# Kernel optimization log

Measured on AMD Instinct MI355X. Metric: run time of the kernel, lower is better.

Reference implementation:

```python
import jax, jax.numpy as jnp
import numpy as np

HEAD = 128
BLOCK = 16
MAX_POS = 32768


def _rope_cache(dim=HEAD, base=10000.0, max_pos=MAX_POS):
    # Mirrors PrecomputedRotaryEmbedding: inv_freq/t in bf16, then cos/sin.
    inv = (1.0 / base ** (jnp.arange(0, dim, 2, dtype=jnp.float32) / dim)).astype(jnp.bfloat16)
    t = jnp.arange(max_pos, dtype=jnp.bfloat16)
    freqs = t[:, None] * inv[None, :]                      # [P, dim/2]
    emb = jnp.concatenate([freqs, freqs], axis=-1)         # [P, dim]
    return jnp.cos(emb).astype(jnp.float32), jnp.sin(emb).astype(jnp.float32)


def _rotary(x, cos, sin):
    # x: [B, H, D], cos/sin: [B, D]
    d2 = x.shape[-1] // 2
    rot = jnp.concatenate([-x[..., d2:], x[..., :d2]], axis=-1)
    return x * cos[:, None, :] + rot * sin[:, None, :]


def setup_inputs() -> dict:
    key = jax.random.key(0)
    ks = jax.random.split(key, 8)
    B, H, Hkv, D = 32, 32, 8, 128
    blocks_per_seq, bs = 128, BLOCK
    nblk = B * blocks_per_seq
    query = jax.random.normal(ks[0], (B, H, D), dtype=jnp.float32)
    k_new = jax.random.normal(ks[1], (B, Hkv, D), dtype=jnp.float32)
    v_new = jax.random.normal(ks[2], (B, Hkv, D), dtype=jnp.float32)
    k_cache = jax.random.normal(ks[3], (nblk, bs, Hkv, D), dtype=jnp.float32)
    v_cache = jax.random.normal(ks[4], (nblk, bs, Hkv, D), dtype=jnp.float32)
    block_table = jnp.arange(nblk, dtype=jnp.int32).reshape(B, blocks_per_seq)
    context_lens = jax.random.randint(ks[5], (B,), 1, 2048, dtype=jnp.int32)
    return {"query": query, "key": k_new, "value": v_new,
            "k_cache": k_cache, "v_cache": v_cache,
            "block_table": block_table, "context_lens": context_lens}


def reference(query, key, value, k_cache, v_cache, block_table, context_lens):
    B, H, D = query.shape
    Hkv = key.shape[1]
    nblk, bs, _, _ = k_cache.shape
    max_ctx = block_table.shape[1] * bs

    cos_c, sin_c = _rope_cache(dim=D)
    pos = context_lens.astype(jnp.int32)
    cos, sin = cos_c[pos], sin_c[pos]                      # [B, D]
    q = _rotary(query, cos, sin)                           # [B, H, D]
    k_new = _rotary(key, cos, sin)                         # [B, Hkv, D]

    # Scatter new k/v into the paged cache at slot of token (ctx - 1).
    last = pos - 1
    slot = block_table[jnp.arange(B), last // bs] * bs + last % bs  # [B]
    kf = k_cache.reshape(nblk * bs, Hkv, D).at[slot].set(k_new)
    vf = v_cache.reshape(nblk * bs, Hkv, D).at[slot].set(value)

    # Gather per-sequence KV via block table (irregular paged access).
    t = jnp.arange(max_ctx)
    idx = block_table[:, t // bs].astype(jnp.int32) * bs + (t % bs)[None, :].astype(jnp.int32)  # [B, L]
    idx = jnp.clip(idx, 0, nblk * bs - 1)
    K = kf[idx]                                            # [B, L, Hkv, D]
    V = vf[idx]

    scale = D ** -0.5
    g = H // Hkv
    qg = q.reshape(B, Hkv, g, D)
    scores = jnp.einsum('bkgd,blkd->bkgl', qg, K) * scale  # [B, Hkv, g, L]
    valid = t[None, :] < pos[:, None]                      # [B, L]
    scores = jnp.where(valid[:, None, None, :], scores, -1e30)
    p = jax.nn.softmax(scores, axis=-1)
    out = jnp.einsum('bkgl,blkd->bkgd', p, V)              # [B, Hkv, g, D]
    return out.reshape(B, H, D)
```

## Files before the change

### kernel.cpp

```cpp
#include <hip/hip_runtime.h>
#include <hip/hip_bf16.h>
#include <math.h>

#define NB 32
#define NH 32
#define HKV 8
#define GQ 4
#define DH 128
#define BS 16
#define BPS 128
#define MAXC 2048
#define NSPLIT 8
#define TILE 32
#define PART_STRIDE 520

__device__ __forceinline__ float bf16r(float x) {
    return __bfloat162float(__float2bfloat16(x));
}

__global__ void rope_kernel(const float* __restrict__ q,
                            const float* __restrict__ knew,
                            const int* __restrict__ ctx,
                            float* __restrict__ q_rot,
                            float* __restrict__ k_rot)
{
    int b = blockIdx.x;
    int d = threadIdx.x;
    int pos = ctx[b];
    int i2 = d & 63;
    float e  = (float)i2 * (1.0f / 64.0f);
    float pf = (float)pow(10000.0, (double)e);
    float inv = bf16r(1.0f / pf);
    float tb  = bf16r((float)pos);
    float fr  = bf16r(tb * inv);
    float c   = bf16r(cosf(fr));
    float s   = bf16r(sinf(fr));

    const float* qb = q + (size_t)b * NH * DH;
    float* qo = q_rot + (size_t)b * NH * DH;
    #pragma unroll 4
    for (int h = 0; h < NH; ++h) {
        float x  = qb[h * DH + d];
        float xr = (d < 64) ? -qb[h * DH + d + 64] : qb[h * DH + d - 64];
        qo[h * DH + d] = x * c + xr * s;
    }
    const float* kb = knew + (size_t)b * HKV * DH;
    float* ko = k_rot + (size_t)b * HKV * DH;
    #pragma unroll
    for (int h = 0; h < HKV; ++h) {
        float x  = kb[h * DH + d];
        float xr = (d < 64) ? -kb[h * DH + d + 64] : kb[h * DH + d - 64];
        ko[h * DH + d] = x * c + xr * s;
    }
}

__global__ void rowidx_kernel(const int* __restrict__ bt,
                              const int* __restrict__ ctx,
                              int* __restrict__ rowidx)
{
    __shared__ int slot_l[NB];
    int tid = threadIdx.x;
    if (tid < NB) {
        int last = ctx[tid] - 1;
        slot_l[tid] = bt[tid * BPS + (last >> 4)] * BS + (last & 15);
    }
    __syncthreads();
    int g = blockIdx.x * 256 + tid;
    int b = g >> 11;
    int t = g & (MAXC - 1);
    int flat = bt[b * BPS + (t >> 4)] * BS + (t & 15);
    int o = flat;
    #pragma unroll
    for (int j = 0; j < NB; ++j)
        if (flat == slot_l[j]) o = -(j + 1);
    rowidx[g] = o;
}

__global__ __launch_bounds__(256) void attn_partial(
    const float* __restrict__ kc, const float* __restrict__ vc,
    const float* __restrict__ vnew,
    const int* __restrict__ ctx,
    const float* __restrict__ q_rot, const float* __restrict__ k_rot,
    const int* __restrict__ rowidx, float* __restrict__ part)
{
    __shared__ float q_lds[GQ][DH];
    __shared__ float k_lds[TILE][DH];
    __shared__ float v_lds[TILE][DH];
    __shared__ float p_lds[GQ][TILE];

    int tid = threadIdx.x;
    int bid = blockIdx.x;
    int sp  = bid & (NSPLIT - 1);
    int kvh = (bid / NSPLIT) & (HKV - 1);
    int b   = bid / (NSPLIT * HKV);

    int L = ctx[b];
    int chunk = (L + NSPLIT - 1) / NSPLIT;
    int start = sp * chunk;
    int end   = min(L, start + chunk);

    {
        const float* qs = q_rot + ((size_t)b * NH + kvh * GQ) * DH;
        ((float*)q_lds)[tid]       = qs[tid];
        ((float*)q_lds)[tid + 256] = qs[tid + 256];
    }

    int lane = tid & 63;
    int h    = tid >> 6;
    int l    = lane & 31;
    int half = lane >> 5;
    int rr   = tid >> 5;
    int c4   = tid & 31;

    float  m_run = -INFINITY;
    float  s_run = 0.0f;
    float2 acc   = make_float2(0.f, 0.f);

    float4 k0, k1, k2, k3, v0, v1, v2, v3;

#define GATHER(T, KD, VD)                                                   \
    {                                                                        \
        int tt = min((T), end - 1);                                          \
        int o  = rowidx[(b << 11) | tt];                                     \
        int j  = -o - 1;                                                     \
        const float* kp = (o >= 0) ? kc + (size_t)o * (HKV * DH) + kvh * DH  \
                                   : k_rot + ((size_t)j * HKV + kvh) * DH;   \
        const float* vp = (o >= 0) ? vc + (size_t)o * (HKV * DH) + kvh * DH  \
                                   : vnew + ((size_t)j * HKV + kvh) * DH;    \
        KD = ((const float4*)kp)[c4];                                        \
        VD = ((const float4*)vp)[c4];                                        \
    }

#define PREFETCH(TB)                    \
    GATHER((TB) + rr,      k0, v0);     \
    GATHER((TB) + rr + 8,  k1, v1);     \
    GATHER((TB) + rr + 16, k2, v2);     \
    GATHER((TB) + rr + 24, k3, v3);

#define LDS_WRITE(TB)                                                        \
    {                                                                        \
        if ((TB) + rr < end) {                                               \
            int sc = (c4 ^ rr) * 4;                                          \
            *(float4*)&k_lds[rr][sc] = k0; *(float4*)&v_lds[rr][sc] = v0;    \
        }                                                                    \
        if ((TB) + rr + 8 < end) {                                           \
            int sc = (c4 ^ (rr + 8)) * 4;                                    \
            *(float4*)&k_lds[rr + 8][sc] = k1; *(float4*)&v_lds[rr + 8][sc] = v1; \
        }                                                                    \
        if ((TB) + rr + 16 < end) {                                          \
            int sc = (c4 ^ (rr + 16)) * 4;                                   \
            *(float4*)&k_lds[rr + 16][sc] = k2; *(float4*)&v_lds[rr + 16][sc] = v2; \
        }                                                                    \
        if ((TB) + rr + 24 < end) {                                          \
            int sc = (c4 ^ (rr + 24)) * 4;                                   \
            *(float4*)&k_lds[rr + 24][sc] = k3; *(float4*)&v_lds[rr + 24][sc] = v3; \
        }                                                                    \
    }

    PREFETCH(start);
    __syncthreads();

    for (int t0 = start; t0 < end; t0 += TILE) {
        int n = min(TILE, end - t0);

        LDS_WRITE(t0);
        __syncthreads();

        PREFETCH(t0 + TILE);

        float s = 0.f;
        if (l < n) {
            const float4* qrow = (const float4*)q_lds[h];
            #pragma unroll
            for (int k = 0; k < 16; ++k) {
                int j = half * 16 + k;
                float4 a  = qrow[j];
                float4 bb = *(const float4*)&k_lds[l][(j ^ l) * 4];
                s += a.x * bb.x + a.y * bb.y + a.z * bb.z + a.w * bb.w;
            }
        }
        s += __shfl_xor(s, 32);
        s *= 0.08838834764831845f;

        float sm = (l < n) ? s : -INFINITY;
        float tm = sm;
        #pragma unroll
        for (int off = 16; off >= 1; off >>= 1)
            tm = fmaxf(tm, __shfl_xor(tm, off));
        float mnew = fmaxf(m_run, tm);
        float p  = (l < n) ? expf(s - mnew) : 0.f;
        float ts = p;
        #pragma unroll
        for (int off = 16; off >= 1; off >>= 1)
            ts += __shfl_xor(ts, off);
        float r = expf(m_run - mnew);
        s_run = s_run * r + ts;
        m_run = mnew;
        acc.x *= r; acc.y *= r;
        if (half == 0) p_lds[h][l] = p;

        int jc = lane >> 1, sub = lane & 1;
        for (int ll = 0; ll < n; ++ll) {
            float pv = p_lds[h][ll];
            const float2 vv = *(const float2*)&v_lds[ll][((jc ^ ll) << 2) + sub * 2];
            acc.x += pv * vv.x;
            acc.y += pv * vv.y;
        }
        __syncthreads();
    }

    float* pp = part + (size_t)bid * PART_STRIDE + h * 130;
    if (lane == 0) { pp[0] = m_run; pp[1] = s_run; }
    *(float2*)&pp[2 + lane * 2] = acc;
}

__global__ void reduce_kernel(const float* __restrict__ part,
                              float* __restrict__ out)
{
    int blk = blockIdx.x;
    int d   = threadIdx.x;
    int b   = blk >> 5;
    int hq  = blk & 31;
    int kvh = hq >> 2;
    int g   = hq & 3;
    const float* base = part + ((size_t)(b * HKV + kvh) * NSPLIT) * PART_STRIDE + g * 130;

    float M = -INFINITY;
    #pragma unroll
    for (int s = 0; s < NSPLIT; ++s)
        M = fmaxf(M, base[(size_t)s * PART_STRIDE]);
    float S = 0.f, o = 0.f;
    #pragma unroll
    for (int s = 0; s < NSPLIT; ++s) {
        float ms = base[(size_t)s * PART_STRIDE];
        float f  = expf(ms - M);
        S += base[(size_t)s * PART_STRIDE + 1] * f;
        o += base[(size_t)s * PART_STRIDE + 2 + d] * f;
    }
    out[(size_t)blk * DH + d] = o / S;
}

extern "C" void kernel_launch(void* const* d_in, const int* in_sizes, int n_in,
                              void* d_out, int out_size, void* d_ws, size_t ws_size,
                              hipStream_t stream)
{
    const float* q    = (const float*)d_in[0];
    const float* knew = (const float*)d_in[1];
    const float* vnew = (const float*)d_in[2];
    const float* kc   = (const float*)d_in[3];
    const float* vc   = (const float*)d_in[4];
    const int*   bt   = (const int*)d_in[5];
    const int*   ctx  = (const int*)d_in[6];
    float* out = (float*)d_out;

    float* ws     = (float*)d_ws;
    float* q_rot  = ws;
    float* k_rot  = ws + 131072;
    int*   rowidx = (int*)(ws + 131072 + 32768);
    float* part   = ws + 131072 + 32768 + 65536;

    rope_kernel<<<NB, 128, 0, stream>>>(q, knew, ctx, q_rot, k_rot);
    rowidx_kernel<<<NB * MAXC / 256, 256, 0, stream>>>(bt, ctx, rowidx);
    attn_partial<<<NB * HKV * NSPLIT, 256, 0, stream>>>(
        kc, vc, vnew, ctx, q_rot, k_rot, rowidx, part);
    reduce_kernel<<<NB * NH, 128, 0, stream>>>(part, out);
}
```

Measured before the change: 78.62 us.

## Fuse rope and rowidx kernels, double split count, shrink tiles, use nontemporal gathers

```diff
diff --git a/kernel.cpp b/kernel.cpp
--- a/kernel.cpp
+++ b/kernel.cpp
@@ -10,62 +10,34 @@
 #define BS 16
 #define BPS 128
 #define MAXC 2048
-#define NSPLIT 8
-#define TILE 32
-#define PART_STRIDE 520
+#define NSPLIT 16
+#define TILE 16
+#define HSTR 132
+#define PART_STRIDE (GQ * HSTR)
+
+typedef __attribute__((ext_vector_type(4))) float f32x4;
 
 __device__ __forceinline__ float bf16r(float x) {
     return __bfloat162float(__float2bfloat16(x));
 }
 
-__global__ void rope_kernel(const float* __restrict__ q,
+__global__ void prep_kernel(const float* __restrict__ q,
                             const float* __restrict__ knew,
+                            const int* __restrict__ bt,
                             const int* __restrict__ ctx,
                             float* __restrict__ q_rot,
-                            float* __restrict__ k_rot)
-{
-    int b = blockIdx.x;
-    int d = threadIdx.x;
-    int pos = ctx[b];
-    int i2 = d & 63;
-    float e  = (float)i2 * (1.0f / 64.0f);
-    float pf = (float)pow(10000.0, (double)e);
-    float inv = bf16r(1.0f / pf);
-    float tb  = bf16r((float)pos);
-    float fr  = bf16r(tb * inv);
-    float c   = bf16r(cosf(fr));
-    float s   = bf16r(sinf(fr));
-
-    const float* qb = q + (size_t)b * NH * DH;
-    float* qo = q_rot + (size_t)b * NH * DH;
-    #pragma unroll 4
-    for (int h = 0; h < NH; ++h) {
-        float x  = qb[h * DH + d];
-        float xr = (d < 64) ? -qb[h * DH + d + 64] : qb[h * DH + d - 64];
-        qo[h * DH + d] = x * c + xr * s;
-    }
-    const float* kb = knew + (size_t)b * HKV * DH;
-    float* ko = k_rot + (size_t)b * HKV * DH;
-    #pragma unroll
-    for (int h = 0; h < HKV; ++h) {
-        float x  = kb[h * DH + d];
-        float xr = (d < 64) ? -kb[h * DH + d + 64] : kb[h * DH + d - 64];
-        ko[h * DH + d] = x * c + xr * s;
-    }
-}
-
-__global__ void rowidx_kernel(const int* __restrict__ bt,
-                              const int* __restrict__ ctx,
-                              int* __restrict__ rowidx)
+                            float* __restrict__ k_rot,
+                            int* __restrict__ rowidx)
 {
     __shared__ int slot_l[NB];
-    int tid = threadIdx.x;
+    int tid = threadIdx.x, bid = blockIdx.x;
     if (tid < NB) {
         int last = ctx[tid] - 1;
         slot_l[tid] = bt[tid * BPS + (last >> 4)] * BS + (last & 15);
     }
     __syncthreads();
-    int g = blockIdx.x * 256 + tid;
+
+    int g = bid * 256 + tid;
     int b = g >> 11;
     int t = g & (MAXC - 1);
     int flat = bt[b * BPS + (t >> 4)] * BS + (t & 15);
@@ -74,9 +46,41 @@
     for (int j = 0; j < NB; ++j)
         if (flat == slot_l[j]) o = -(j + 1);
     rowidx[g] = o;
-}
-
-__global__ __launch_bounds__(256) void attn_partial(
+
+    if (bid < NB) {
+        int rb  = bid;
+        int d   = tid & 127;
+        int hi  = tid >> 7;
+        int pos = ctx[rb];
+        int i2  = d & 63;
+        float e   = (float)i2 * (1.0f / 64.0f);
+        float pf  = (float)pow(10000.0, (double)e);
+        float inv = bf16r(1.0f / pf);
+        float tb  = bf16r((float)pos);
+        float fr  = bf16r(tb * inv);
+        float c   = bf16r(cosf(fr));
+        float s   = bf16r(sinf(fr));
+
+        const float* qb = q + (size_t)rb * NH * DH;
+        float* qo = q_rot + (size_t)rb * NH * DH;
+        #pragma unroll 4
+        for (int h = hi * 16; h < hi * 16 + 16; ++h) {
+            float x  = qb[h * DH + d];
+            float xr = (d < 64) ? -qb[h * DH + d + 64] : qb[h * DH + d - 64];
+            qo[h * DH + d] = x * c + xr * s;
+        }
+        const float* kb = knew + (size_t)rb * HKV * DH;
+        float* ko = k_rot + (size_t)rb * HKV * DH;
+        #pragma unroll
+        for (int h = hi * 4; h < hi * 4 + 4; ++h) {
+            float x  = kb[h * DH + d];
+            float xr = (d < 64) ? -kb[h * DH + d + 64] : kb[h * DH + d - 64];
+            ko[h * DH + d] = x * c + xr * s;
+        }
+    }
+}
+
+__global__ __launch_bounds__(256, 8) void attn_partial(
     const float* __restrict__ kc, const float* __restrict__ vc,
     const float* __restrict__ vnew,
     const int* __restrict__ ctx,
@@ -90,9 +94,9 @@
 
     int tid = threadIdx.x;
     int bid = blockIdx.x;
-    int sp  = bid & (NSPLIT - 1);
-    int kvh = (bid / NSPLIT) & (HKV - 1);
-    int b   = bid / (NSPLIT * HKV);
+    int b   = bid & 31;
+    int kvh = (bid >> 5) & 7;
+    int sp  = bid >> 8;
 
     int L = ctx[b];
     int chunk = (L + NSPLIT - 1) / NSPLIT;
@@ -107,8 +111,8 @@
 
     int lane = tid & 63;
     int h    = tid >> 6;
-    int l    = lane & 31;
-    int half = lane >> 5;
+    int l    = lane & 15;
+    int quad = lane >> 4;
     int rr   = tid >> 5;
     int c4   = tid & 31;
 
@@ -116,88 +120,73 @@
     float  s_run = 0.0f;
     float2 acc   = make_float2(0.f, 0.f);
 
-    float4 k0, k1, k2, k3, v0, v1, v2, v3;
-
-#define GATHER(T, KD, VD)                                                   \
+    f32x4 k0, k1, v0, v1;
+
+#define GATHER(T, KD, VD)                                                    \
     {                                                                        \
         int tt = min((T), end - 1);                                          \
-        int o  = rowidx[(b << 11) | tt];                                     \
-        int j  = -o - 1;                                                     \
-        const float* kp = (o >= 0) ? kc + (size_t)o * (HKV * DH) + kvh * DH  \
-                                   : k_rot + ((size_t)j * HKV + kvh) * DH;   \
-        const float* vp = (o >= 0) ? vc + (size_t)o * (HKV * DH) + kvh * DH  \
-                                   : vnew + ((size_t)j * HKV + kvh) * DH;    \
-        KD = ((const float4*)kp)[c4];                                        \
-        VD = ((const float4*)vp)[c4];                                        \
-    }
-
-#define PREFETCH(TB)                    \
-    GATHER((TB) + rr,      k0, v0);     \
-    GATHER((TB) + rr + 8,  k1, v1);     \
-    GATHER((TB) + rr + 16, k2, v2);     \
-    GATHER((TB) + rr + 24, k3, v3);
-
-#define LDS_WRITE(TB)                                                        \
-    {                                                                        \
-        if ((TB) + rr < end) {                                               \
-            int sc = (c4 ^ rr) * 4;                                          \
-            *(float4*)&k_lds[rr][sc] = k0; *(float4*)&v_lds[rr][sc] = v0;    \
-        }                                                                    \
-        if ((TB) + rr + 8 < end) {                                           \
-            int sc = (c4 ^ (rr + 8)) * 4;                                    \
-            *(float4*)&k_lds[rr + 8][sc] = k1; *(float4*)&v_lds[rr + 8][sc] = v1; \
-        }                                                                    \
-        if ((TB) + rr + 16 < end) {                                          \
-            int sc = (c4 ^ (rr + 16)) * 4;                                   \
-            *(float4*)&k_lds[rr + 16][sc] = k2; *(float4*)&v_lds[rr + 16][sc] = v2; \
-        }                                                                    \
-        if ((TB) + rr + 24 < end) {                                          \
-            int sc = (c4 ^ (rr + 24)) * 4;                                   \
-            *(float4*)&k_lds[rr + 24][sc] = k3; *(float4*)&v_lds[rr + 24][sc] = v3; \
-        }                                                                    \
-    }
-
-    PREFETCH(start);
+        int o  = __builtin_nontemporal_load(rowidx + ((b << 11) | tt));      \
+        size_t off = (o >= 0) ? (size_t)o * (HKV * DH) + kvh * DH            \
+                              : ((size_t)(-o - 1) * HKV + kvh) * DH;         \
+        const f32x4* kp = (const f32x4*)(((o >= 0) ? kc : k_rot) + off);     \
+        const f32x4* vp = (const f32x4*)(((o >= 0) ? vc : vnew) + off);      \
+        KD = __builtin_nontemporal_load(kp + c4);                            \
+        VD = __builtin_nontemporal_load(vp + c4);                            \
+    }
+
+    GATHER(start + rr,     k0, v0);
+    GATHER(start + rr + 8, k1, v1);
     __syncthreads();
 
     for (int t0 = start; t0 < end; t0 += TILE) {
         int n = min(TILE, end - t0);
 
-        LDS_WRITE(t0);
+        if (t0 + rr < end) {
+            int sc = (c4 ^ rr) * 4;
+            *(f32x4*)&k_lds[rr][sc] = k0;
+            *(f32x4*)&v_lds[rr][sc] = v0;
+        }
+        if (t0 + rr + 8 < end) {
+            int sc = (c4 ^ (rr + 8)) * 4;
+            *(f32x4*)&k_lds[rr + 8][sc] = k1;
+            *(f32x4*)&v_lds[rr + 8][sc] = v1;
+        }
         __syncthreads();
 
-        PREFETCH(t0 + TILE);
+        GATHER(t0 + TILE + rr,     k0, v0);
+        GATHER(t0 + TILE + rr + 8, k1, v1);
 
         float s = 0.f;
         if (l < n) {
             const float4* qrow = (const float4*)q_lds[h];
             #pragma unroll
-            for (int k = 0; k < 16; ++k) {
-                int j = half * 16 + k;
+            for (int k = 0; k < 8; ++k) {
+                int j = quad * 8 + k;
                 float4 a  = qrow[j];
                 float4 bb = *(const float4*)&k_lds[l][(j ^ l) * 4];
                 s += a.x * bb.x + a.y * bb.y + a.z * bb.z + a.w * bb.w;
             }
         }
+        s += __shfl_xor(s, 16);
         s += __shfl_xor(s, 32);
         s *= 0.08838834764831845f;
 
         float sm = (l < n) ? s : -INFINITY;
         float tm = sm;
         #pragma unroll
-        for (int off = 16; off >= 1; off >>= 1)
+        for (int off = 8; off >= 1; off >>= 1)
             tm = fmaxf(tm, __shfl_xor(tm, off));
         float mnew = fmaxf(m_run, tm);
-        float p  = (l < n) ? expf(s - mnew) : 0.f;
+        float p  = (l < n) ? __expf(s - mnew) : 0.f;
         float ts = p;
         #pragma unroll
-        for (int off = 16; off >= 1; off >>= 1)
+        for (int off = 8; off >= 1; off >>= 1)
             ts += __shfl_xor(ts, off);
-        float r = expf(m_run - mnew);
+        float r = __expf(m_run - mnew);
         s_run = s_run * r + ts;
         m_run = mnew;
         acc.x *= r; acc.y *= r;
-        if (half == 0) p_lds[h][l] = p;
+        if (lane < TILE) p_lds[h][l] = p;
 
         int jc = lane >> 1, sub = lane & 1;
         for (int ll = 0; ll < n; ++ll) {
@@ -209,9 +198,10 @@
         __syncthreads();
     }
 
-    float* pp = part + (size_t)bid * PART_STRIDE + h * 130;
-    if (lane == 0) { pp[0] = m_run; pp[1] = s_run; }
-    *(float2*)&pp[2 + lane * 2] = acc;
+    float* pp = part + (size_t)((b * HKV + kvh) * NSPLIT + sp) * PART_STRIDE
+              + h * HSTR;
+    *(float2*)&pp[lane * 2] = acc;
+    if (lane == 0) { pp[128] = m_run; pp[129] = s_run; }
 }
 
 __global__ void reduce_kernel(const float* __restrict__ part,
@@ -223,21 +213,22 @@
     int hq  = blk & 31;
     int kvh = hq >> 2;
     int g   = hq & 3;
-    const float* base = part + ((size_t)(b * HKV + kvh) * NSPLIT) * PART_STRIDE + g * 130;
+    const float* base = part + (size_t)((b * HKV + kvh) * NSPLIT) * PART_STRIDE
+                      + g * HSTR;
 
     float M = -INFINITY;
     #pragma unroll
     for (int s = 0; s < NSPLIT; ++s)
-        M = fmaxf(M, base[(size_t)s * PART_STRIDE]);
-    float S = 0.f, o = 0.f;
+        M = fmaxf(M, base[(size_t)s * PART_STRIDE + 128]);
+    float S = 0.f, acc = 0.f;
     #pragma unroll
     for (int s = 0; s < NSPLIT; ++s) {
-        float ms = base[(size_t)s * PART_STRIDE];
-        float f  = expf(ms - M);
-        S += base[(size_t)s * PART_STRIDE + 1] * f;
-        o += base[(size_t)s * PART_STRIDE + 2 + d] * f;
-    }
-    out[(size_t)blk * DH + d] = o / S;
+        float ms = base[(size_t)s * PART_STRIDE + 128];
+        float f  = __expf(ms - M);
+        S   += base[(size_t)s * PART_STRIDE + 129] * f;
+        acc += base[(size_t)s * PART_STRIDE + d] * f;
+    }
+    out[(size_t)blk * DH + d] = acc / S;
 }
 
 extern "C" void kernel_launch(void* const* d_in, const int* in_sizes, int n_in,
@@ -259,8 +250,8 @@
     int*   rowidx = (int*)(ws + 131072 + 32768);
     float* part   = ws + 131072 + 32768 + 65536;
 
-    rope_kernel<<<NB, 128, 0, stream>>>(q, knew, ctx, q_rot, k_rot);
-    rowidx_kernel<<<NB * MAXC / 256, 256, 0, stream>>>(bt, ctx, rowidx);
+    prep_kernel<<<NB * MAXC / 256, 256, 0, stream>>>(q, knew, bt, ctx,
+                                                     q_rot, k_rot, rowidx);
     attn_partial<<<NB * HKV * NSPLIT, 256, 0, stream>>>(
         kc, vc, vnew, ctx, q_rot, k_rot, rowidx, part);
     reduce_kernel<<<NB * NH, 128, 0, stream>>>(part, out);
```

Result: slower. 129.6 us (+64.9%).
